# Kernel optimization log

Hardware: AMD Instinct MI355X
Metric: run time of the kernel (lower is better)

## Reference

```python
import jax, jax.numpy as jnp
import numpy as np
import math

B, D, N, T, H = 16, 64, 200, 48, 8
DK = D // H
EPS = 1e-5


def layer_norm(x, g, b):
    m = jnp.mean(x, axis=-1, keepdims=True)
    v = jnp.var(x, axis=-1, keepdims=True)
    return (x - m) * jax.lax.rsqrt(v + EPS) * g + b


def conv1x3(x, w, b):
    # x: (B, D, N, T), w: (D, D, 1, 3) 'same' padding along T
    y = jax.lax.conv_general_dilated(
        x, w, window_strides=(1, 1), padding=((0, 0), (1, 1)),
        dimension_numbers=('NCHW', 'OIHW', 'NCHW'))
    return y + b[None, :, None, None]


def setup_inputs() -> dict:
    key = jax.random.key(0)
    ks = jax.random.split(key, 12)
    s = 1.0 / math.sqrt(D)
    inp = {
        'x': jax.random.normal(ks[0], (B, D, N, T), jnp.float32),
        'support_matrix': jax.random.uniform(ks[1], (N, N), jnp.float32) / N,
        'Wq': jax.random.normal(ks[2], (D, D, 1, 3), jnp.float32) * s,
        'bq': jnp.zeros((D,), jnp.float32),
        'Wk': jax.random.normal(ks[3], (D, D, 1, 3), jnp.float32) * s,
        'bk': jnp.zeros((D,), jnp.float32),
        'W1': jax.random.normal(ks[4], (D, D), jnp.float32) * s,
        'b1': jnp.zeros((D,), jnp.float32),
        'W2': jax.random.normal(ks[5], (D, D), jnp.float32) * s,
        'b2': jnp.zeros((D,), jnp.float32),
        'Theta': jax.random.normal(ks[6], (D, D), jnp.float32) * s,
        'g0': jnp.ones((D,), jnp.float32),
        'beta0': jnp.zeros((D,), jnp.float32),
        'g1': jnp.ones((D,), jnp.float32),
        'beta1': jnp.zeros((D,), jnp.float32),
    }
    return inp


def temporal_attn(x, Wq, bq, Wk, bk, W1, b1, W2, b2):
    # x: (B, D, N, T)
    q = conv1x3(x, Wq, bq).reshape(B, H, DK, N, T).transpose(0, 3, 1, 4, 2)  # (B,N,h,T,dk)
    k = conv1x3(x, Wk, bk).reshape(B, H, DK, N, T).transpose(0, 3, 1, 4, 2)
    xp = x.transpose(0, 2, 3, 1)  # (B,N,T,D)
    v = (xp @ W1.T + b1).reshape(B, N, T, H, DK).transpose(0, 1, 3, 2, 4)  # (B,N,h,T,dk)
    scores = jnp.einsum('bnhtd,bnhsd->bnhts', q, k) / math.sqrt(DK)
    p = jax.nn.softmax(scores, axis=-1)
    out = jnp.einsum('bnhts,bnhsd->bnhtd', p, v)
    out = out.transpose(0, 1, 3, 2, 4).reshape(B, N, T, D)
    return out @ W2.T + b2


def spatial_gcn(x, adj, Theta):
    # x: (B,N,T,D) -> per-timestep spatial attention + adjacency-weighted GCN
    xt = x.transpose(0, 2, 1, 3)  # (B,T,N,D)
    score = jnp.einsum('btnf,btmf->btnm', xt, xt) / math.sqrt(D)
    att = jax.nn.softmax(score, axis=-1) / math.sqrt(D)
    agg = jnp.einsum('btnm,btmf->btnf', adj[None, None] * att, xt)
    out = jax.nn.relu(agg @ Theta.T)  # (B,T,N,D)
    return out.transpose(0, 2, 1, 3)  # (B,N,T,D)


def reference(x, support_matrix, Wq, bq, Wk, bk, W1, b1, W2, b2, Theta,
              g0, beta0, g1, beta1):
    t_out = temporal_attn(x, Wq, bq, Wk, bk, W1, b1, W2, b2)
    h = x.transpose(0, 2, 3, 1) + layer_norm(t_out, g0, beta0)  # (B,N,T,D)
    s_out = spatial_gcn(h, support_matrix, Theta)
    return h + layer_norm(s_out, g1, beta1)
```

## Files before the change

### kernel.cpp

```cpp
#include <hip/hip_runtime.h>
#include <hip/hip_bf16.h>

typedef unsigned short u16t;

namespace {

constexpr int kB = 16, kD = 64, kN = 200, kT = 48, kH = 8;
constexpr float kEps = 1e-5f;

typedef __attribute__((ext_vector_type(8))) __bf16 bf16x8;
typedef __attribute__((ext_vector_type(4))) float f32x4;
union B8 { int4 i; bf16x8 v; u16t u[8]; };

__device__ __forceinline__ u16t f2bfu(float f) {
  union { __hip_bfloat16 h; u16t u; } c; c.h = __float2bfloat16(f); return c.u;
}
__device__ __forceinline__ unsigned pk2(float a, float b) {
  return (unsigned)f2bfu(a) | ((unsigned)f2bfu(b) << 16);
}

constexpr int kWqOff = 0;
constexpr int kWkOff = 12288;
constexpr int kW1Off = 24576;
constexpr int kW2Off = 28672;
constexpr int kThOff = 32768;
constexpr size_t kWsWeightBytes = 73728;
constexpr size_t kHBytes = (size_t)kB * kN * kT * kD * 4;

__global__ void k0_prep(const float* __restrict__ Wq, const float* __restrict__ Wk,
                        const float* __restrict__ W1, const float* __restrict__ W2,
                        const float* __restrict__ Theta, u16t* __restrict__ ws) {
  const int tid = blockIdx.x * 256 + threadIdx.x;
  const int stride = gridDim.x * 256;
  for (int idx = tid; idx < 64 * 192; idx += stride) {
    const int row = idx / 192, rem = idx % 192;
    const int tap = rem >> 6, c = rem & 63;
    const int src = row * 192 + c * 3 + tap;
    ws[kWqOff + idx] = f2bfu(Wq[src]);
    ws[kWkOff + idx] = f2bfu(Wk[src]);
  }
  for (int idx = tid; idx < 4096; idx += stride) {
    ws[kW1Off + idx] = f2bfu(W1[idx]);
    ws[kW2Off + idx] = f2bfu(W2[idx]);
    ws[kThOff + idx] = f2bfu(Theta[idx]);
  }
}

__global__ __launch_bounds__(256, 4) void k1_temporal(
    const float* __restrict__ x, const u16t* __restrict__ ws,
    const float* __restrict__ bq, const float* __restrict__ bk,
    const float* __restrict__ b1, const float* __restrict__ b2,
    const float* __restrict__ g0, const float* __restrict__ beta0,
    float* __restrict__ hout)
{
  __shared__ __align__(16) float qs[3072];
  __shared__ __align__(16) u16t lds_h[13440];
  u16t* XT  = lds_h;
  u16t* osT = lds_h;
  u16t* QT  = lds_h + 3200;
  u16t* KT  = lds_h + 6272;
  u16t* VTT = lds_h + 9344;

  const int tid = threadIdx.x;
  const int b = blockIdx.x / kN, n = blockIdx.x % kN;
  const int wv = tid >> 6, lane = tid & 63;
  const int c15 = lane & 15, quad = lane >> 4;

  if (tid < 192) {
    const int dp = tid & 31, j = tid >> 5;
    const int d0 = dp * 2;
    const size_t xi = (size_t)b * (kD*kN*kT) + (size_t)d0 * (kN*kT) + (size_t)n * kT + j * 8;
    const float4 a0 = *(const float4*)(x + xi);
    const float4 a1 = *(const float4*)(x + xi + 4);
    const float4 c0 = *(const float4*)(x + xi + kN*kT);
    const float4 c1 = *(const float4*)(x + xi + kN*kT + 4);
    float f0[8] = {a0.x,a0.y,a0.z,a0.w,a1.x,a1.y,a1.z,a1.w};
    float f1[8] = {c0.x,c0.y,c0.z,c0.w,c1.x,c1.y,c1.z,c1.w};
    u16t* bb = XT + (d0 & 7);
    const int blk = d0 >> 3;
    #pragma unroll
    for (int e = 0; e < 8; ++e) {
      const int r = j*8 + e + 1;
      const unsigned pkd = (unsigned)f2bfu(f0[e]) | ((unsigned)f2bfu(f1[e]) << 16);
      *(unsigned*)(bb + r*64 + ((blk + r) & 7) * 8) = pkd;
    }
  } else if (tid < 208) {
    const int g = tid - 192;
    const int rr = (g >> 3) ? 49 : 0, gg = g & 7;
    *(int4*)(XT + rr*64 + gg*8) = make_int4(0,0,0,0);
  }
  if (tid < 128) {
    const int d = tid >> 1, g = tid & 1;
    *(int4*)(VTT + d*64 + (((6 + g + d) & 7) << 3)) = make_int4(0,0,0,0);
  }
  __syncthreads();

  {
    const int dqr = wv*16 + c15;
    B8 aq[6], ak[6], av2[2];
    #pragma unroll
    for (int tap = 0; tap < 3; ++tap)
      #pragma unroll
      for (int ksp = 0; ksp < 2; ++ksp) {
        const int off = dqr*192 + tap*64 + ksp*32 + quad*8;
        aq[tap*2+ksp].i = *(const int4*)(ws + kWqOff + off);
        ak[tap*2+ksp].i = *(const int4*)(ws + kWkOff + off);
      }
    #pragma unroll
    for (int ksp = 0; ksp < 2; ++ksp)
      av2[ksp].i = *(const int4*)(ws + kW1Off + dqr*64 + ksp*32 + quad*8);
    float bqv[4], bkv[4], b1v[4];
    #pragma unroll
    for (int r = 0; r < 4; ++r) {
      const int row = wv*16 + quad*4 + r;
      bqv[r] = bq[row]; bkv[r] = bk[row]; b1v[r] = b1[row];
    }
    const int dbase = wv*16 + quad*4;
    const int dblk = dbase >> 3;
    constexpr float kScale = 0.35355339059327373f;

    for (int i = 0; i < 3; ++i) {
      const int t0 = i * 16;
      B8 bf[3][2];
      #pragma unroll
      for (int tap = 0; tap < 3; ++tap)
        #pragma unroll
        for (int ksp = 0; ksp < 2; ++ksp) {
          const int r = t0 + c15 + tap;
          bf[tap][ksp].i = *(const int4*)(XT + r*64 + (((ksp*4 + quad) + r) & 7)*8);
        }
      f32x4 accq = {0.f,0.f,0.f,0.f}, acck = {0.f,0.f,0.f,0.f}, accv = {0.f,0.f,0.f,0.f};
      #pragma unroll
      for (int tap = 0; tap < 3; ++tap)
        #pragma unroll
        for (int ksp = 0; ksp < 2; ++ksp) {
          accq = __builtin_amdgcn_mfma_f32_16x16x32_bf16(aq[tap*2+ksp].v, bf[tap][ksp].v, accq, 0, 0, 0);
          acck = __builtin_amdgcn_mfma_f32_16x16x32_bf16(ak[tap*2+ksp].v, bf[tap][ksp].v, acck, 0, 0, 0);
        }
      #pragma unroll
      for (int ksp = 0; ksp < 2; ++ksp)
        accv = __builtin_amdgcn_mfma_f32_16x16x32_bf16(av2[ksp].v, bf[1][ksp].v, accv, 0, 0, 0);

      const int t = t0 + c15;
      const int rotq = (dblk + t) & 7;
      const unsigned q01 = pk2((accq[0]+bqv[0])*kScale, (accq[1]+bqv[1])*kScale);
      const unsigned q23 = pk2((accq[2]+bqv[2])*kScale, (accq[3]+bqv[3])*kScale);
      *(int2*)(QT + t*64 + rotq*8 + (quad&1)*4) = make_int2((int)q01, (int)q23);
      const unsigned k01 = pk2(acck[0]+bkv[0], acck[1]+bkv[1]);
      const unsigned k23 = pk2(acck[2]+bkv[2], acck[3]+bkv[3]);
      *(int2*)(KT + t*64 + rotq*8 + (quad&1)*4) = make_int2((int)k01, (int)k23);
      #pragma unroll
      for (int r = 0; r < 4; ++r) {
        const int d = dbase + r;
        VTT[d*64 + ((((t>>3) + d) & 7) << 3) + (t & 7)] = f2bfu(accv[r] + b1v[r]);
      }
    }
  }
  __syncthreads();

  #pragma unroll
  for (int hh = 0; hh < 2; ++hh) {
    const int h = wv*2 + hh;
    B8 vb[2];
    #pragma unroll
    for (int ksp = 0; ksp < 2; ++ksp) {
      if (c15 < 8) {
        const int dr = h*8 + c15;
        vb[ksp].i = *(const int4*)(VTT + dr*64 + (((ksp*4 + quad + dr) & 7) << 3));
      } else vb[ksp].i = make_int4(0,0,0,0);
    }
    #pragma unroll
    for (int nt = 0; nt < 3; ++nt) {
      B8 qb;
      if (quad == 0) {
        const int t = nt*16 + c15;
        qb.i = *(const int4*)(QT + t*64 + (((h + t) & 7) << 3));
      } else qb.i = make_int4(0,0,0,0);
      f32x4 sa[3];
      #pragma unroll
      for (int ms = 0; ms < 3; ++ms) {
        B8 ka;
        if (quad == 0) {
          const int s = ms*16 + c15;
          ka.i = *(const int4*)(KT + s*64 + (((h + s) & 7) << 3));
        } else ka.i = make_int4(0,0,0,0);
        f32x4 z = {0.f,0.f,0.f,0.f};
        sa[ms] = __builtin_amdgcn_mfma_f32_16x16x32_bf16(ka.v, qb.v, z, 0, 0, 0);
      }
      float p[3][4]; float es = 0.f;
      #pragma unroll
      for (int ms = 0; ms < 3; ++ms)
        #pragma unroll
        for (int r = 0; r < 4; ++r) { p[ms][r] = __expf(sa[ms][r]); es += p[ms][r]; }
      es += __shfl_xor(es, 16, 64);
      es += __shfl_xor(es, 32, 64);
      const float inv = __fdividef(1.f, es);
      unsigned pkk[3][2];
      #pragma unroll
      for (int ms = 0; ms < 3; ++ms) {
        pkk[ms][0] = pk2(p[ms][0]*inv, p[ms][1]*inv);
        pkk[ms][1] = pk2(p[ms][2]*inv, p[ms][3]*inv);
      }
      const int srcA = c15 + ((2*(quad & 1)) << 4);
      const int srcB = srcA + 16;
      const unsigned w0A = __shfl((int)pkk[0][0], srcA, 64), w0B = __shfl((int)pkk[1][0], srcA, 64);
      const unsigned w1A = __shfl((int)pkk[0][1], srcA, 64), w1B = __shfl((int)pkk[1][1], srcA, 64);
      const unsigned w2A = __shfl((int)pkk[0][0], srcB, 64), w2B = __shfl((int)pkk[1][0], srcB, 64);
      const unsigned w3A = __shfl((int)pkk[0][1], srcB, 64), w3B = __shfl((int)pkk[1][1], srcB, 64);
      const bool hi = quad >= 2;
      B8 a0;
      a0.i = make_int4((int)(hi ? w0B : w0A), (int)(hi ? w1B : w1A),
                       (int)(hi ? w2B : w2A), (int)(hi ? w3B : w3A));
      const int srcC = (c15 + ((2*quad) << 4)) & 63;
      const int srcD = (srcC + 16) & 63;
      const unsigned y0 = __shfl((int)pkk[2][0], srcC, 64), y1 = __shfl((int)pkk[2][1], srcC, 64);
      const unsigned y2 = __shfl((int)pkk[2][0], srcD, 64), y3 = __shfl((int)pkk[2][1], srcD, 64);
      B8 a1;
      if (quad < 2) a1.i = make_int4((int)y0, (int)y1, (int)y2, (int)y3);
      else          a1.i = make_int4(0,0,0,0);
      f32x4 ov = {0.f,0.f,0.f,0.f};
      ov = __builtin_amdgcn_mfma_f32_16x16x32_bf16(a0.v, vb[0].v, ov, 0, 0, 0);
      ov = __builtin_amdgcn_mfma_f32_16x16x32_bf16(a1.v, vb[1].v, ov, 0, 0, 0);
      if (c15 < 8) {
        #pragma unroll
        for (int r = 0; r < 4; ++r) {
          const int t = nt*16 + quad*4 + r;
          osT[t*64 + (((h + t) & 7) << 3) + c15] = f2bfu(ov[r]);
        }
      }
    }
  }
  __syncthreads();

  {
    const int dqr = wv*16 + c15;
    B8 a2[2];
    #pragma unroll
    for (int ksp = 0; ksp < 2; ++ksp)
      a2[ksp].i = *(const int4*)(ws + kW2Off + dqr*64 + ksp*32 + quad*8);
    float b2v[4];
    #pragma unroll
    for (int r = 0; r < 4; ++r) b2v[r] = b2[wv*16 + quad*4 + r];
    for (int i = 0; i < 3; ++i) {
      const int t0 = i * 16;
      f32x4 acc = {0.f,0.f,0.f,0.f};
      #pragma unroll
      for (int ksp = 0; ksp < 2; ++ksp) {
        const int r = t0 + c15;
        B8 bo; bo.i = *(const int4*)(osT + r*64 + (((ksp*4 + quad) + r) & 7)*8);
        acc = __builtin_amdgcn_mfma_f32_16x16x32_bf16(a2[ksp].v, bo.v, acc, 0, 0, 0);
      }
      #pragma unroll
      for (int r = 0; r < 4; ++r)
        qs[(wv*16 + quad*4 + r)*48 + t0 + c15] = acc[r] + b2v[r];
    }
  }
  __syncthreads();

  float* redm = reinterpret_cast<float*>(lds_h);
  float* redv = redm + 192;
  float* mrs  = redm + 384;
  float* rrs  = redm + 432;
  if (tid < 192) {
    const int t = tid >> 2, grp = tid & 3;
    float sm = 0.f, sq = 0.f;
    #pragma unroll
    for (int i = 0; i < 16; ++i) {
      const float v = qs[(grp*16+i)*48 + t];
      sm += v; sq += v*v;
    }
    redm[t*4+grp] = sm; redv[t*4+grp] = sq;
  }
  __syncthreads();
  if (tid < 48) {
    const int t = tid;
    const float sm = redm[t*4] + redm[t*4+1] + redm[t*4+2] + redm[t*4+3];
    const float sq = redv[t*4] + redv[t*4+1] + redv[t*4+2] + redv[t*4+3];
    const float mean = sm * (1.f/64.f);
    const float var = sq * (1.f/64.f) - mean*mean;
    mrs[t] = mean; rrs[t] = rsqrtf(fmaxf(var, 0.f) + kEps);
  }
  __syncthreads();
  if (tid < 192) {
    const int t = tid >> 2, grp = tid & 3;
    const float mean = mrs[t], rs = rrs[t];
    const size_t base = (((size_t)b*kN + n)*kT + t)*kD + grp*16;
    const float* xp = x + (size_t)b*(kD*kN*kT) + (size_t)n*kT + t;
    #pragma unroll
    for (int i4 = 0; i4 < 4; ++i4) {
      float4 o;
      float* op = (float*)&o;
      #pragma unroll
      for (int e = 0; e < 4; ++e) {
        const int d = grp*16 + i4*4 + e;
        const float tout = qs[d*48 + t];
        const float xv = xp[(size_t)d * (kN*kT)];
        op[e] = xv + (tout - mean)*rs*g0[d] + beta0[d];
      }
      *(float4*)(hout + base + i4*4) = o;
    }
  }
}

__global__ __launch_bounds__(256, 4) void k2_spatial_mfma(
    const float* __restrict__ hsrc, float* __restrict__ hdst,
    const float* __restrict__ adj, const u16t* __restrict__ ws,
    const float* __restrict__ g1, const float* __restrict__ beta1, int nparts)
{
  __shared__ __align__(16) u16t Hs[208*64];
  __shared__ __align__(16) u16t Wb[16*224];
  __shared__ __align__(16) u16t A2[16*64];
  __shared__ float rsum[4][16], lnS[4][16], lnQ[4][16];

  const int tid = threadIdx.x;
  int bt, part;
  if (nparts == 2) { bt = blockIdx.x >> 1; part = blockIdx.x & 1; }
  else             { bt = blockIdx.x;      part = 0; }
  const int b = bt / kT, t = bt % kT;
  const int rbBeg = (part == 0) ? 0 : 7;
  const int rbEnd = (nparts == 2 && part == 0) ? 7 : 13;
  const int wv = tid >> 6, lane = tid & 63;
  const int c15 = lane & 15, quad = lane >> 4;
  const int myf = wv*16 + c15;

  const float g1f = g1[myf], be1f = beta1[myf];

  B8 bth[2];
  #pragma unroll
  for (int ksp = 0; ksp < 2; ++ksp)
    bth[ksp].i = *(const int4*)(ws + kThOff + myf*64 + ksp*32 + quad*8);

  for (int idx = tid; idx < kN*8; idx += 256) {
    const int n = idx >> 3, j = idx & 7;
    const float* src = hsrc + (((size_t)b*kN + n)*kT + t)*kD + j*8;
    const float4 p0 = *(const float4*)src, p1 = *(const float4*)(src + 4);
    B8 p;
    p.u[0]=f2bfu(p0.x); p.u[1]=f2bfu(p0.y); p.u[2]=f2bfu(p0.z); p.u[3]=f2bfu(p0.w);
    p.u[4]=f2bfu(p1.x); p.u[5]=f2bfu(p1.y); p.u[6]=f2bfu(p1.z); p.u[7]=f2bfu(p1.w);
    *(int4*)(Hs + n*64 + (((j + n) & 7) << 3)) = p.i;
  }
  if (tid < 64) {
    *(int4*)(Hs + (200 + (tid >> 3))*64 + ((tid & 7) << 3)) = make_int4(0,0,0,0);
  }
  for (int idx = tid; idx < (16*224)/8; idx += 256)
    *(int4*)(Wb + idx*8) = make_int4(0,0,0,0);
  __syncthreads();

  const int dA = wv*16 + c15;
  B8 ahi[7];
  #pragma unroll
  for (int ksp = 0; ksp < 6; ++ksp) {
    const int m0 = ksp*32 + quad*8;
    #pragma unroll
    for (int j = 0; j < 8; ++j) {
      const int m = m0 + j;
      ahi[ksp].u[j] = Hs[m*64 + ((((dA>>3) + m) & 7) << 3) + (dA & 7)];
    }
  }
  if (quad == 0) {
    #pragma unroll
    for (int j = 0; j < 8; ++j) {
      const int m = 192 + j;
      ahi[6].u[j] = Hs[m*64 + ((((dA>>3) + m) & 7) << 3) + (dA & 7)];
    }
  } else {
    ahi[6].i = make_int4(0, 0, 0, 0);
  }

  for (int rb = rbBeg; rb < rbEnd; ++rb) {
    const int n0 = rb * 16;
    const bool has4 = (wv == 0);

    float adjv[3][4], adj3[4];
    #pragma unroll
    for (int r = 0; r < 4; ++r) {
      const int n = n0 + quad*4 + r;
      const bool vrow = (n < kN);
      const int na = vrow ? n : (kN - 1);
      #pragma unroll
      for (int i = 0; i < 3; ++i) {
        const int m = (wv + 4*i)*16 + c15;
        adjv[i][r] = vrow ? adj[(size_t)na*kN + m] : 0.f;
      }
      adj3[r] = (has4 && c15 < 8 && vrow) ? adj[(size_t)na*kN + 192 + c15] : 0.f;
    }

    B8 afr[2];
    #pragma unroll
    for (int ksp = 0; ksp < 2; ++ksp) {
      const int row = n0 + c15;
      afr[ksp].i = *(const int4*)(Hs + row*64 + (((ksp*4 + quad + row) & 7) << 3));
    }
    f32x4 cs[3];
    #pragma unroll
    for (int i = 0; i < 3; ++i) {
      const int mt = wv + 4*i;
      f32x4 acc = {0.f, 0.f, 0.f, 0.f};
      #pragma unroll
      for (int ksp = 0; ksp < 2; ++ksp) {
        const int row = mt*16 + c15;
        B8 bfr; bfr.i = *(const int4*)(Hs + row*64 + (((ksp*4 + quad + row) & 7) << 3));
        acc = __builtin_amdgcn_mfma_f32_16x16x32_bf16(afr[ksp].v, bfr.v, acc, 0, 0, 0);
      }
      cs[i] = acc;
    }
    f32x4 cs3 = {0.f, 0.f, 0.f, 0.f};
    if (has4) {
      #pragma unroll
      for (int ksp = 0; ksp < 2; ++ksp) {
        const int row = 192 + c15;
        B8 bfr; bfr.i = *(const int4*)(Hs + row*64 + (((ksp*4 + quad + row) & 7) << 3));
        cs3 = __builtin_amdgcn_mfma_f32_16x16x32_bf16(afr[ksp].v, bfr.v, cs3, 0, 0, 0);
      }
    }

    float smr[4];
    #pragma unroll
    for (int r = 0; r < 4; ++r) {
      cs[0][r] = __expf(fmaf(cs[0][r], 0.125f, -20.f));
      cs[1][r] = __expf(fmaf(cs[1][r], 0.125f, -20.f));
      cs[2][r] = __expf(fmaf(cs[2][r], 0.125f, -20.f));
      cs3[r]   = (has4 && c15 < 8) ? __expf(fmaf(cs3[r], 0.125f, -20.f)) : 0.f;
      smr[r] = cs[0][r] + cs[1][r] + cs[2][r] + cs3[r];
    }
    #pragma unroll
    for (int off = 1; off <= 8; off <<= 1)
      #pragma unroll
      for (int r = 0; r < 4; ++r) smr[r] += __shfl_xor(smr[r], off, 64);
    if (c15 == 0) {
      #pragma unroll
      for (int r = 0; r < 4; ++r) rsum[wv][quad*4 + r] = smr[r];
    }
    __syncthreads();
    #pragma unroll
    for (int r = 0; r < 4; ++r) {
      const int rr = quad*4 + r;
      const float tot = rsum[0][rr] + rsum[1][rr] + rsum[2][rr] + rsum[3][rr];
      const float inv = __fdividef(0.125f, fmaxf(tot, 1e-30f));
      #pragma unroll
      for (int i = 0; i < 3; ++i) {
        const int m = (wv + 4*i)*16 + c15;
        const float w = cs[i][r] * inv * adjv[i][r];
        Wb[rr*224 + (((m >> 3) + rr) % 28)*8 + (m & 7)] = f2bfu(w);
      }
      if (has4 && c15 < 8) {
        const int m = 192 + c15;
        const float w = cs3[r] * inv * adj3[r];
        Wb[rr*224 + (((m >> 3) + rr) % 28)*8 + (m & 7)] = f2bfu(w);
      }
    }
    __syncthreads();

    f32x4 ag = {0.f, 0.f, 0.f, 0.f};
    #pragma unroll
    for (int ksp = 0; ksp < 7; ++ksp) {
      B8 bw; bw.i = *(const int4*)(Wb + c15*224 + ((ksp*4 + quad + c15) % 28)*8);
      ag = __builtin_amdgcn_mfma_f32_16x16x32_bf16(ahi[ksp].v, bw.v, ag, 0, 0, 0);
    }
    {
      const int dbase = wv*16 + quad*4;
      #pragma unroll
      for (int r = 0; r < 4; ++r) {
        const int d = dbase + r;
        A2[c15*64 + (((d >> 3) + c15) & 7)*8 + (d & 7)] = f2bfu(ag[r]);
      }
    }
    __syncthreads();

    f32x4 o = {0.f, 0.f, 0.f, 0.f};
    #pragma unroll
    for (int ksp = 0; ksp < 2; ++ksp) {
      B8 a; a.i = *(const int4*)(A2 + c15*64 + (((ksp*4 + quad + c15) & 7) << 3));
      o = __builtin_amdgcn_mfma_f32_16x16x32_bf16(a.v, bth[ksp].v, o, 0, 0, 0);
    }
    float vr[4], ps[4], pq[4];
    #pragma unroll
    for (int r = 0; r < 4; ++r) {
      vr[r] = fmaxf(o[r], 0.f);
      ps[r] = vr[r]; pq[r] = vr[r]*vr[r];
    }
    #pragma unroll
    for (int off = 1; off <= 8; off <<= 1)
      #pragma unroll
      for (int r = 0; r < 4; ++r) {
        ps[r] += __shfl_xor(ps[r], off, 64);
        pq[r] += __shfl_xor(pq[r], off, 64);
      }
    if (c15 == 0) {
      #pragma unroll
      for (int r = 0; r < 4; ++r) { lnS[wv][quad*4+r] = ps[r]; lnQ[wv][quad*4+r] = pq[r]; }
    }
    __syncthreads();
    #pragma unroll
    for (int r = 0; r < 4; ++r) {
      const int rr = quad*4 + r, n = n0 + rr;
      const float S = lnS[0][rr] + lnS[1][rr] + lnS[2][rr] + lnS[3][rr];
      const float Q = lnQ[0][rr] + lnQ[1][rr] + lnQ[2][rr] + lnQ[3][rr];
      const float mean = S * (1.f/64.f);
      const float var = Q * (1.f/64.f) - mean*mean;
      const float rs = rsqrtf(fmaxf(var, 0.f) + kEps);
      if (n < kN) {
        const float sout = (vr[r] - mean)*rs*g1f + be1f;
        const size_t oi = (((size_t)b*kN + n)*kT + t)*kD + myf;
        hdst[oi] = hsrc[oi] + sout;
      }
    }
  }
}

}

extern "C" void kernel_launch(void* const* d_in, const int* in_sizes, int n_in,
                              void* d_out, int out_size, void* d_ws, size_t ws_size,
                              hipStream_t stream) {
  const float* x     = (const float*)d_in[0];
  const float* adj   = (const float*)d_in[1];
  const float* Wq    = (const float*)d_in[2];
  const float* bq    = (const float*)d_in[3];
  const float* Wk    = (const float*)d_in[4];
  const float* bk    = (const float*)d_in[5];
  const float* W1    = (const float*)d_in[6];
  const float* b1    = (const float*)d_in[7];
  const float* W2    = (const float*)d_in[8];
  const float* b2    = (const float*)d_in[9];
  const float* Theta = (const float*)d_in[10];
  const float* g0    = (const float*)d_in[11];
  const float* beta0 = (const float*)d_in[12];
  const float* g1    = (const float*)d_in[13];
  const float* beta1 = (const float*)d_in[14];

  u16t* wsb = (u16t*)d_ws;

  const bool split = ws_size >= kWsWeightBytes + kHBytes;
  float* hbuf = split ? (float*)((char*)d_ws + kWsWeightBytes) : (float*)d_out;
  const int nparts = split ? 2 : 1;

  k0_prep<<<dim3(48), dim3(256), 0, stream>>>(Wq, Wk, W1, W2, Theta, wsb);
  k1_temporal<<<dim3(kB*kN), dim3(256), 0, stream>>>(
      x, wsb, bq, bk, b1, b2, g0, beta0, hbuf);
  k2_spatial_mfma<<<dim3(kB*kT*nparts), dim3(256), 0, stream>>>(
      hbuf, (float*)d_out, adj, wsb, g1, beta1, nparts);
}
```

Measured before the change: 251.2 us.

## Stage residual x tile in LDS with coalesced loads; split spatial kernel four ways

In the temporal kernel, the residual x values are now loaded with coalesced float4 reads along T into a padded LDS tile. The LN-stats threads run concurrently with this load, replacing strided per-element global reads in the output loop. The spatial kernel's row-block range is split across four blocks per (b,t) instead of two, which raises grid parallelism. The cost is redundant per-block setup (H staging, softmax over full N) repeated across more blocks.

```diff
diff --git a/kernel.cpp b/kernel.cpp
--- a/kernel.cpp
+++ b/kernel.cpp
@@ -261,6 +261,7 @@
   float* redv = redm + 192;
   float* mrs  = redm + 384;
   float* rrs  = redm + 432;
+  float* xs   = reinterpret_cast<float*>(lds_h + 3200);
   if (tid < 192) {
     const int t = tid >> 2, grp = tid & 3;
     float sm = 0.f, sq = 0.f;
@@ -272,8 +273,24 @@
     redm[t*4+grp] = sm; redv[t*4+grp] = sq;
   }
   __syncthreads();
-  if (tid < 48) {
-    const int t = tid;
+  if (tid < 192) {
+    const int dp = tid & 31, j = tid >> 5;
+    const int d0 = dp * 2;
+    const size_t xi = (size_t)b * (kD*kN*kT) + (size_t)d0 * (kN*kT) + (size_t)n * kT + j * 8;
+    const float4 a0 = *(const float4*)(x + xi);
+    const float4 a1 = *(const float4*)(x + xi + 4);
+    const float4 c0 = *(const float4*)(x + xi + kN*kT);
+    const float4 c1 = *(const float4*)(x + xi + kN*kT + 4);
+    float f0[8] = {a0.x,a0.y,a0.z,a0.w,a1.x,a1.y,a1.z,a1.w};
+    float f1[8] = {c0.x,c0.y,c0.z,c0.w,c1.x,c1.y,c1.z,c1.w};
+    #pragma unroll
+    for (int e = 0; e < 8; ++e) {
+      xs[d0*49 + j*8 + e]       = f0[e];
+      xs[(d0+1)*49 + j*8 + e]   = f1[e];
+    }
+  }
+  if (tid >= 192 && tid < 240) {
+    const int t = tid - 192;
     const float sm = redm[t*4] + redm[t*4+1] + redm[t*4+2] + redm[t*4+3];
     const float sq = redv[t*4] + redv[t*4+1] + redv[t*4+2] + redv[t*4+3];
     const float mean = sm * (1.f/64.f);
@@ -285,7 +302,6 @@
     const int t = tid >> 2, grp = tid & 3;
     const float mean = mrs[t], rs = rrs[t];
     const size_t base = (((size_t)b*kN + n)*kT + t)*kD + grp*16;
-    const float* xp = x + (size_t)b*(kD*kN*kT) + (size_t)n*kT + t;
     #pragma unroll
     for (int i4 = 0; i4 < 4; ++i4) {
       float4 o;
@@ -294,7 +310,7 @@
       for (int e = 0; e < 4; ++e) {
         const int d = grp*16 + i4*4 + e;
         const float tout = qs[d*48 + t];
-        const float xv = xp[(size_t)d * (kN*kT)];
+        const float xv = xs[d*49 + t];
         op[e] = xv + (tout - mean)*rs*g0[d] + beta0[d];
       }
       *(float4*)(hout + base + i4*4) = o;
@@ -313,12 +329,18 @@
   __shared__ float rsum[4][16], lnS[4][16], lnQ[4][16];
 
   const int tid = threadIdx.x;
-  int bt, part;
-  if (nparts == 2) { bt = blockIdx.x >> 1; part = blockIdx.x & 1; }
-  else             { bt = blockIdx.x;      part = 0; }
+  int bt, part, rbBeg, rbEnd;
+  if (nparts == 4) {
+    bt = blockIdx.x >> 2; part = blockIdx.x & 3;
+    rbBeg = (part == 0) ? 0 : 4 + 3*(part - 1);
+    rbEnd = rbBeg + ((part == 0) ? 4 : 3);
+  } else if (nparts == 2) {
+    bt = blockIdx.x >> 1; part = blockIdx.x & 1;
+    rbBeg = part ? 7 : 0; rbEnd = part ? 13 : 7;
+  } else {
+    bt = blockIdx.x; rbBeg = 0; rbEnd = 13;
+  }
   const int b = bt / kT, t = bt % kT;
-  const int rbBeg = (part == 0) ? 0 : 7;
-  const int rbEnd = (nparts == 2 && part == 0) ? 7 : 13;
   const int wv = tid >> 6, lane = tid & 63;
   const int c15 = lane & 15, quad = lane >> 4;
   const int myf = wv*16 + c15;
@@ -533,7 +555,7 @@
 
   const bool split = ws_size >= kWsWeightBytes + kHBytes;
   float* hbuf = split ? (float*)((char*)d_ws + kWsWeightBytes) : (float*)d_out;
-  const int nparts = split ? 2 : 1;
+  const int nparts = split ? 4 : 1;
 
   k0_prep<<<dim3(48), dim3(256), 0, stream>>>(Wq, Wk, W1, W2, Theta, wsb);
   k1_temporal<<<dim3(kB*kN), dim3(256), 0, stream>>>(
```

Measured after the change: 256.4 us. 1.02x slower.
